# Performance work log

Measured on AMD Instinct MI355X. Metric: run time of the kernel, lower is better.

Reference implementation:

```python
import jax, jax.numpy as jnp
import numpy as np

B, T, NE, H = 4, 1024, 1024, 16
HS = NE // H  # 64
EPS = 0.00064


def setup_inputs() -> dict:
    key = jax.random.key(0)
    ks = jax.random.split(key, 30)
    def rn(k, shape, s):
        return jax.random.normal(k, shape, jnp.float32) * s
    d = {}
    d["x"] = jax.random.normal(ks[0], (B, T, NE), jnp.float32)
    d["time_maa_x"] = jax.random.uniform(ks[1], (NE,), jnp.float32)
    d["time_maa"] = jax.random.uniform(ks[2], (4, 1, 1, NE), jnp.float32)
    d["maa_w1"] = rn(ks[3], (128, NE), 0.02)   # 4 * D_MIX_LORA=32
    d["maa_w2"] = rn(ks[4], (4, 32, NE), 0.02)
    d["decay_w1"] = rn(ks[5], (64, NE), 0.02)
    d["decay_w2"] = rn(ks[6], (64, NE), 0.02)
    d["aaa_w1"] = rn(ks[7], (16, NE), 0.02)
    d["aaa_w2"] = rn(ks[8], (16, NE), 0.02)
    d["kkk_w1"] = rn(ks[9], (16, NE), 0.02)
    d["kkk_w2"] = rn(ks[10], (16, NE), 0.02)
    d["gate_w1"] = rn(ks[11], (128, NE), 0.02)
    d["gate_w2"] = rn(ks[12], (128, NE), 0.02)
    d["ma_w1"] = rn(ks[13], (16, NE), 0.02)
    d["ma_w2"] = rn(ks[14], (16, NE), 0.02)
    d["mk_w1"] = rn(ks[15], (16, NE), 0.02)
    d["mk_w2"] = rn(ks[16], (16, NE), 0.02)
    d["time_decay"] = jnp.linspace(-6.5, -1.5, NE, dtype=jnp.float32)  # decay_speed + 0.5 shape
    d["time_faaaa"] = rn(ks[17], (NE,), 0.02)
    d["time_aaaaa"] = rn(ks[18], (NE,), 0.02)
    d["time_misc_a"] = rn(ks[19], (NE,), 0.02)
    d["time_misc_k"] = rn(ks[20], (NE,), 0.02)
    d["Wr"] = rn(ks[21], (NE, NE), 0.5 / NE ** 0.5)
    d["Wk"] = rn(ks[22], (NE, NE), 0.05 / NE ** 0.5)
    d["Wv"] = rn(ks[23], (NE, NE), 0.5 / NE ** 0.5)
    d["Wo"] = rn(ks[24], (NE, NE), 1.0 / NE ** 0.5)
    d["ln_w"] = jnp.ones((NE,), jnp.float32)
    d["ln_b"] = jnp.zeros((NE,), jnp.float32)
    return d


def _forward(x, time_maa_x, time_maa, maa_w1, maa_w2, decay_w1, decay_w2,
             aaa_w1, aaa_w2, kkk_w1, kkk_w2, gate_w1, gate_w2,
             ma_w1, ma_w2, mk_w1, mk_w2, time_decay, time_faaaa, time_aaaaa,
             time_misc_a, time_misc_k, Wr, Wk, Wv, Wo, ln_w, ln_b):
    Bx, Tx, C = x.shape
    # token-shift delta: xx[t] = x[t-1] - x[t], with x[-1] = 0
    xx = jnp.pad(x, ((0, 0), (1, 0), (0, 0)))[:, :Tx] - x
    mix = x + xx * time_maa_x
    lo = jnp.tanh(jnp.einsum('btc,dc->btd', mix, maa_w1)).reshape(Bx, Tx, 4, 32)
    lo = jnp.einsum('btgk,gkc->gbtc', lo, maa_w2)           # [4,B,T,C]
    xm = x[None] + xx[None] * (lo + time_maa)               # time_maa broadcasts [4,1,1,C]
    xrg, xwa, xk, xv = xm[0], xm[1], xm[2], xm[3]

    r = xrg @ Wr.T
    g = jnp.tanh(xrg @ gate_w1.T) @ gate_w2
    k = xk @ Wk.T
    v = xv @ Wv.T
    w2 = jnp.tanh(xwa @ decay_w1.T) @ decay_w2
    w = -jax.nn.softplus(-(time_decay + w2)) - 0.5
    kk = k + jnp.tanh(xk @ kkk_w1.T) @ kkk_w2
    kkh = kk.reshape(Bx, Tx, H, HS)
    kk = (kkh / jnp.maximum(jnp.linalg.norm(kkh, axis=-1, keepdims=True), 1e-12)).reshape(Bx, Tx, C)
    a = jax.nn.sigmoid(time_aaaaa + (xwa @ aaa_w1.T) @ aaa_w2)
    ma = jax.nn.sigmoid(time_misc_a + (xwa @ ma_w1.T) @ ma_w2)
    k = k * ma + k * a * (1.0 - ma)
    mk = jax.nn.sigmoid(time_misc_k + (xk @ mk_w1.T) @ mk_w2)
    k = k * jnp.exp(w * mk)
    b = -kk * a

    # RWKV7 delta-rule recurrence: per-(B,H) HSxHS matrix state, scan over T
    def to_th(t):
        return t.reshape(Bx, Tx, H, HS).transpose(1, 0, 2, 3)  # [T,B,H,HS]
    qt, wt, kt, vt, at, bt = map(to_th, (r, w, k, v, kk, b))
    wt = jnp.exp(-jnp.exp(wt))

    def step(s, inp):
        q_, w_, k_, v_, a_, b_ = inp
        sa = jnp.einsum('bhij,bhj->bhi', s, a_)
        s = s * w_[:, :, None, :] + sa[..., None] * b_[:, :, None, :] + v_[..., None] * k_[:, :, None, :]
        return s, jnp.einsum('bhij,bhj->bhi', s, q_)

    s0 = jnp.zeros((Bx, H, HS, HS), x.dtype)
    _, y = jax.lax.scan(step, s0, (qt, wt, kt, vt, at, bt))
    y = y.transpose(1, 0, 2, 3).reshape(Bx, Tx, C)

    # GroupNorm with H groups, eps=0.00064
    yg = y.reshape(Bx, Tx, H, HS)
    mu = yg.mean(-1, keepdims=True)
    var = ((yg - mu) ** 2).mean(-1, keepdims=True)
    y = ((yg - mu) / jnp.sqrt(var + EPS)).reshape(Bx, Tx, C) * ln_w + ln_b

    # per-head bonus: (r.k * faaaa) v
    rk = (r.reshape(Bx, Tx, H, HS) * k.reshape(Bx, Tx, H, HS) * time_faaaa.reshape(H, HS)).sum(-1, keepdims=True)
    y = y + (rk * v.reshape(Bx, Tx, H, HS)).reshape(Bx, Tx, C)
    return (y * g) @ Wo.T


def reference(x, time_maa_x, time_maa, maa_w1, maa_w2, decay_w1, decay_w2,
              aaa_w1, aaa_w2, kkk_w1, kkk_w2, gate_w1, gate_w2,
              ma_w1, ma_w2, mk_w1, mk_w2, time_decay, time_faaaa, time_aaaaa,
              time_misc_a, time_misc_k, Wr, Wk, Wv, Wo, ln_w, ln_b):
    return _forward(x, time_maa_x, time_maa, maa_w1, maa_w2, decay_w1, decay_w2,
                    aaa_w1, aaa_w2, kkk_w1, kkk_w2, gate_w1, gate_w2,
                    ma_w1, ma_w2, mk_w1, mk_w2, time_decay, time_faaaa, time_aaaaa,
                    time_misc_a, time_misc_k, Wr, Wk, Wv, Wo, ln_w, ln_b)
```

## Files before the change

### kernel.cpp

```cpp
#include <hip/hip_runtime.h>
#include <cstdint>
#include <cstddef>

#define BB   4
#define TT   1024
#define CC   1024
#define HH   16
#define HSS  64
#define NNtok 4096
#define EPSGN 0.00064f
#define W2TS 192

typedef unsigned short bf16u;
typedef __attribute__((ext_vector_type(8))) short short8;
typedef __attribute__((ext_vector_type(4))) float f32x4;
#define SLOT 4194304ull

__device__ __forceinline__ float bf2f(bf16u u){
  union { unsigned int i; float f; } cv; cv.i = ((unsigned int)u) << 16; return cv.f;
}
__device__ __forceinline__ unsigned short f2bfbits(unsigned int x){
  return (unsigned short)((x + 0x7fffu + ((x >> 16) & 1u)) >> 16);
}
__device__ __forceinline__ bf16u f2bf(float f){
  union { float f; unsigned int i; } cv; cv.f = f;
  return f2bfbits(cv.i);
}
__device__ __forceinline__ void ld4bf(const bf16u* p, float* o){
  ushort4 u = *reinterpret_cast<const ushort4*>(p);
  o[0]=bf2f(u.x); o[1]=bf2f(u.y); o[2]=bf2f(u.z); o[3]=bf2f(u.w);
}
__device__ __forceinline__ void st4bf(bf16u* p, const float* v){
  ushort4 u; u.x=f2bf(v[0]); u.y=f2bf(v[1]); u.z=f2bf(v[2]); u.w=f2bf(v[3]);
  *reinterpret_cast<ushort4*>(p) = u;
}
__device__ __forceinline__ unsigned short f2h(float f){
  union { _Float16 h; unsigned short s; } c; c.h = (_Float16)f; return c.s;
}
__device__ __forceinline__ void st4h(bf16u* p, const float* v){
  ushort4 u; u.x=f2h(v[0]); u.y=f2h(v[1]); u.z=f2h(v[2]); u.w=f2h(v[3]);
  *reinterpret_cast<ushort4*>(p) = u;
}
__device__ __forceinline__ void ld4f(const float* p, float* o){
  float4 v = *reinterpret_cast<const float4*>(p);
  o[0]=v.x; o[1]=v.y; o[2]=v.z; o[3]=v.w;
}
__device__ __forceinline__ float sigm(float x){ return 1.f / (1.f + expf(-x)); }

__device__ __forceinline__ float bflo(unsigned int u){
  union { unsigned int i; float f; } c; c.i = u << 16; return c.f;
}
__device__ __forceinline__ float bfhi(unsigned int u){
  union { unsigned int i; float f; } c; c.i = u & 0xffff0000u; return c.f;
}
__device__ __forceinline__ float hlo(unsigned int u){
  union { unsigned short s; _Float16 h; } c; c.s = (unsigned short)(u & 0xffffu); return (float)c.h;
}
__device__ __forceinline__ float hhi(unsigned int u){
  union { unsigned short s; _Float16 h; } c; c.s = (unsigned short)(u >> 16); return (float)c.h;
}
__device__ __forceinline__ float hval(unsigned short s){
  union { unsigned short s; _Float16 h; } c; c.s = s; return (float)c.h;
}
__device__ __forceinline__ float dot4(const float* x, const float* y){
  return (x[0]*y[0] + x[1]*y[1]) + (x[2]*y[2] + x[3]*y[3]);
}

template<int CTRL>
__device__ __forceinline__ float dpp_add(float v){
  union { float f; int i; } a, b;
  a.f = v;
  b.i = __builtin_amdgcn_update_dpp(0, a.i, CTRL, 0xF, 0xF, true);
  return v + b.f;
}
__device__ __forceinline__ float red16(float v){
  v = dpp_add<0xB1>(v);
  v = dpp_add<0x4E>(v);
  v = dpp_add<0x124>(v);
  v = dpp_add<0x128>(v);
  return v;
}
__device__ __forceinline__ float red32(float v){
  v = red16(v);
  union { float f; int i; } x, y;
  x.f = v; y.f = v;
  asm volatile("" : "+v"(y.i));
  asm volatile("v_permlane16_swap_b32 %0, %1" : "+v"(x.i), "+v"(y.i));
  return x.f + y.f;
}

__global__ __launch_bounds__(256) void k_prep(const float* __restrict__ x,
                                              const float* __restrict__ tmx,
                                              bf16u* __restrict__ MIX){
  int e = (blockIdx.x * 256 + threadIdx.x) * 4;
  int n = e >> 10;
  int c = e & (CC - 1);
  int t = n & (TT - 1);
  float xf[4]; ld4f(x + e, xf);
  float pf[4] = {0.f, 0.f, 0.f, 0.f};
  if (t > 0) ld4f(x + e - CC, pf);
  float tm[4]; ld4f(tmx + c, tm);
  float mv[4];
  #pragma unroll
  for (int i = 0; i < 4; ++i) mv[i] = xf[i] + (pf[i] - xf[i]) * tm[i];
  st4bf(MIX + e, mv);
}

__global__ __launch_bounds__(256) void k_wconv1(
    const float* __restrict__ Wr, const float* __restrict__ Wk,
    const float* __restrict__ Wv,
    const float* __restrict__ maa_w1, const float* __restrict__ gate_w1,
    const float* __restrict__ decay_w1, const float* __restrict__ aaa_w1,
    const float* __restrict__ ma_w1, const float* __restrict__ kkk_w1,
    const float* __restrict__ mk_w1,
    const float* __restrict__ maa_w2, const float* __restrict__ decay_w2,
    bf16u* __restrict__ WrB, bf16u* __restrict__ WkB, bf16u* __restrict__ WvB,
    bf16u* __restrict__ W1B, bf16u* __restrict__ W2TB){
  int blk = blockIdx.x, tid = threadIdx.x;
  if (blk < 3072){
    const float* src = (blk < 1024) ? Wr : (blk < 2048) ? Wk : Wv;
    bf16u* dst = (blk < 1024) ? WrB : (blk < 2048) ? WkB : WvB;
    size_t e = (size_t)(blk & 1023) * 1024 + (size_t)tid * 4;
    float v[4]; ld4f(src + e, v);
    st4bf(dst + e, v);
  } else if (blk < 3456){
    int row = blk - 3072;
    const float* src;
    if      (row < 128) src = maa_w1   + (size_t)row * 1024;
    else if (row < 256) src = gate_w1  + (size_t)(row - 128) * 1024;
    else if (row < 320) src = decay_w1 + (size_t)(row - 256) * 1024;
    else if (row < 336) src = aaa_w1   + (size_t)(row - 320) * 1024;
    else if (row < 352) src = ma_w1    + (size_t)(row - 336) * 1024;
    else if (row < 368) src = kkk_w1   + (size_t)(row - 352) * 1024;
    else                src = mk_w1    + (size_t)(row - 368) * 1024;
    float v[4]; ld4f(src + tid * 4, v);
    st4bf(W1B + (size_t)row * 1024 + tid * 4, v);
  } else {
    int j = blk - 3456;
    const float* src = (j < 128) ? (maa_w2 + (size_t)j * 1024)
                                 : (decay_w2 + (size_t)(j - 128) * 1024);
    for (int c = tid; c < 1024; c += 256)
      W2TB[(size_t)c * W2TS + j] = f2bf(src[c]);
  }
}

__global__ __launch_bounds__(256) void k_wconv2(const float* __restrict__ Wo,
                                                const float* __restrict__ gate_w2,
                                                bf16u* __restrict__ WoB,
                                                bf16u* __restrict__ GW2T){
  int blk = blockIdx.x, tid = threadIdx.x;
  if (blk < 1024){
    size_t e = ((size_t)blk * 256 + tid) * 4;
    float v[4]; ld4f(Wo + e, v);
    st4bf(WoB + e, v);
  } else {
    int c = (blk - 1024) * 2 + (tid >> 7);
    int j = tid & 127;
    GW2T[(size_t)c * 128 + j] = f2bf(gate_w2[(size_t)j * CC + c]);
  }
}

#define B64_ASZ (64*40)
#define B64_BSZ (128*40)
template<bool OB>
__device__ __forceinline__ void gemm_b64_body(const bf16u* __restrict__ X,
                                              const bf16u* __restrict__ WB,
                                              void* __restrict__ OUTv,
                                              int Nd, int Kd, int act_n,
                                              short* __restrict__ As,
                                              short* __restrict__ Bs,
                                              int bn0, int bm0){
  const int tid  = threadIdx.x;
  const int lane = tid & 63;
  const int wv   = tid >> 6;
  const int wm   = wv >> 1, wn = wv & 1;
  const int l15  = lane & 15;
  const int quad = lane >> 4;

  f32x4 acc[2][4];
  #pragma unroll
  for (int mi = 0; mi < 2; ++mi)
    #pragma unroll
    for (int ni = 0; ni < 4; ++ni)
      #pragma unroll
      for (int rg = 0; rg < 4; ++rg) acc[mi][ni][rg] = 0.f;

  const int ra = tid >> 2, ka = (tid & 3) * 8;
  const int rb = tid >> 1, kb = (tid & 1) * 16;
  const bf16u* xsrc = X + (size_t)(bm0 + ra) * Kd;
  const bf16u* wsrc = (bn0 + rb < Nd) ? WB + (size_t)(bn0 + rb) * Kd : nullptr;

  uint4 xa = *(const uint4*)(xsrc + ka);
  uint4 wa = make_uint4(0,0,0,0), wb = wa;
  if (wsrc){
    wa = *(const uint4*)(wsrc + kb);
    wb = *(const uint4*)(wsrc + kb + 8);
  }
  *(uint4*)&As[ra * 40 + ka]      = xa;
  *(uint4*)&Bs[rb * 40 + kb]      = wa;
  *(uint4*)&Bs[rb * 40 + kb + 8]  = wb;
  __syncthreads();

  const int NK = Kd >> 5;
  for (int k = 0; k < NK; ++k){
    const int cur = k & 1;
    if (k + 1 < NK){
      int k0 = (k + 1) << 5;
      xa = *(const uint4*)(xsrc + k0 + ka);
      if (wsrc){
        wa = *(const uint4*)(wsrc + k0 + kb);
        wb = *(const uint4*)(wsrc + k0 + kb + 8);
      }
    }
    short8 af[2], bfg[4];
    #pragma unroll
    for (int mi = 0; mi < 2; ++mi)
      af[mi] = *(const short8*)&As[cur*B64_ASZ + (wm*32 + mi*16 + l15) * 40 + quad*8];
    #pragma unroll
    for (int ni = 0; ni < 4; ++ni)
      bfg[ni] = *(const short8*)&Bs[cur*B64_BSZ + (wn*64 + ni*16 + l15) * 40 + quad*8];
    #pragma unroll
    for (int mi = 0; mi < 2; ++mi)
      #pragma unroll
      for (int ni = 0; ni < 4; ++ni)
        acc[mi][ni] = __builtin_amdgcn_mfma_f32_16x16x32_bf16(af[mi], bfg[ni], acc[mi][ni], 0, 0, 0);
    if (k + 1 < NK){
      const int nxt = cur ^ 1;
      *(uint4*)&As[nxt*B64_ASZ + ra * 40 + ka]     = xa;
      *(uint4*)&Bs[nxt*B64_BSZ + rb * 40 + kb]     = wa;
      *(uint4*)&Bs[nxt*B64_BSZ + rb * 40 + kb + 8] = wb;
      __syncthreads();
    }
  }

  #pragma unroll
  for (int mi = 0; mi < 2; ++mi){
    #pragma unroll
    for (int ni = 0; ni < 4; ++ni){
      int col = bn0 + wn*64 + ni*16 + l15;
      if (col >= Nd) continue;
      #pragma unroll
      for (int rg = 0; rg < 4; ++rg){
        int row = bm0 + wm*32 + mi*16 + quad*4 + rg;
        float v = acc[mi][ni][rg];
        if (col < act_n) v = tanhf(v);
        if (OB) ((bf16u*)OUTv)[(size_t)row * Nd + col] = f2bf(v);
        else    ((float*)OUTv)[(size_t)row * Nd + col] = v;
      }
    }
  }
}

template<bool OB>
__global__ __launch_bounds__(256) void k_gemm_b64(const bf16u* __restrict__ X,
                                                  const bf16u* __restrict__ WB,
                                                  void* __restrict__ OUTv,
                                                  int Nd, int Kd, int act_n){
  __shared__ short As[2*B64_ASZ];
  __shared__ short Bs[2*B64_BSZ];
  gemm_b64_body<OB>(X, WB, OUTv, Nd, Kd, act_n, As, Bs,
                    blockIdx.x * 128, blockIdx.y * 64);
}

__global__ __launch_bounds__(256) void k_gemm_b64_lora(const bf16u* __restrict__ X0,
                                                       const bf16u* __restrict__ X1,
                                                       const bf16u* __restrict__ X2,
                                                       const bf16u* __restrict__ W1B,
                                                       bf16u* __restrict__ GT,
                                                       bf16u* __restrict__ P1,
                                                       bf16u* __restrict__ P2){
  __shared__ short As[2*B64_ASZ];
  __shared__ short Bs[2*B64_BSZ];
  const int z = blockIdx.z;
  const int bm0 = blockIdx.y * 64;
  if (z == 0)
    gemm_b64_body<true>(X0, W1B + 128*1024, GT, 128, CC, 128, As, Bs, 0, bm0);
  else if (z == 1)
    gemm_b64_body<true>(X1, W1B + 256*1024, P1, 96, CC, 64, As, Bs, 0, bm0);
  else
    gemm_b64_body<true>(X2, W1B + 352*1024, P2, 32, CC, 16, As, Bs, 0, bm0);
}

template<int KD, int EP>
__device__ __forceinline__ void gemm_nn_body(const bf16u* __restrict__ A, int lda,
                                             const bf16u* __restrict__ BT, int koff,
                                             bf16u* __restrict__ OUT,
                                             const float* __restrict__ x,
                                             const float* __restrict__ tma_g,
                                             short* __restrict__ As,
                                             short* __restrict__ Bs,
                                             int bn0, int bm0){
  const int tid  = threadIdx.x;
  const int lane = tid & 63;
  const int wv   = tid >> 6;
  const int wm   = wv >> 1, wn = wv & 1;
  const int l15  = lane & 15;
  const int quad = lane >> 4;

  for (int idx = tid; idx < 128 * (KD / 8); idx += 256){
    int r  = idx / (KD / 8);
    int kc = (idx % (KD / 8)) * 8;
    *(uint4*)&As[r * (KD + 8) + kc] =
        *(const uint4*)(A + (size_t)(bm0 + r) * lda + kc);
  }
  for (int idx = tid; idx < 128 * (KD / 8); idx += 256){
    int cc_ = idx / (KD / 8);
    int kc  = (idx % (KD / 8)) * 8;
    *(uint4*)&Bs[cc_ * (KD + 8) + kc] =
        *(const uint4*)(BT + (size_t)(bn0 + cc_) * W2TS + koff + kc);
  }
  __syncthreads();

  f32x4 acc[4][4];
  #pragma unroll
  for (int mi = 0; mi < 4; ++mi)
    #pragma unroll
    for (int ni = 0; ni < 4; ++ni)
      #pragma unroll
      for (int rg = 0; rg < 4; ++rg) acc[mi][ni][rg] = 0.f;

  #pragma unroll
  for (int kk = 0; kk < KD; kk += 32){
    short8 af[4], bfg[4];
    #pragma unroll
    for (int mi = 0; mi < 4; ++mi)
      af[mi] = *(const short8*)&As[(wm*64 + mi*16 + l15) * (KD + 8) + kk + quad*8];
    #pragma unroll
    for (int ni = 0; ni < 4; ++ni)
      bfg[ni] = *(const short8*)&Bs[(wn*64 + ni*16 + l15) * (KD + 8) + kk + quad*8];
    #pragma unroll
    for (int mi = 0; mi < 4; ++mi)
      #pragma unroll
      for (int ni = 0; ni < 4; ++ni)
        acc[mi][ni] = __builtin_amdgcn_mfma_f32_16x16x32_bf16(af[mi], bfg[ni], acc[mi][ni], 0, 0, 0);
  }

  #pragma unroll
  for (int mi = 0; mi < 4; ++mi){
    #pragma unroll
    for (int ni = 0; ni < 4; ++ni){
      int col = bn0 + wn*64 + ni*16 + l15;
      float tm = (EP == 1) ? tma_g[col] : 0.f;
      #pragma unroll
      for (int rg = 0; rg < 4; ++rg){
        int row = bm0 + wm*64 + mi*16 + quad*4 + rg;
        float v = acc[mi][ni][rg];
        if (EP == 1){
          float xv = x[(size_t)row * CC + col];
          float xp = ((row & (TT - 1)) == 0) ? 0.f : x[(size_t)row * CC + col - CC];
          v = xv + (xp - xv) * (v + tm);
        }
        OUT[(size_t)row * CC + col] = f2bf(v);
      }
    }
  }
}

template<int KD, int EP>
__global__ __launch_bounds__(256) void k_gemm_nn_b(const bf16u* __restrict__ A, int lda,
                                                   const bf16u* __restrict__ BT, int koff,
                                                   bf16u* __restrict__ OUT,
                                                   const float* __restrict__ x,
                                                   const float* __restrict__ tma_g){
  __shared__ short As[128 * (KD + 8)];
  __shared__ short Bs[128 * (KD + 8)];
  gemm_nn_body<KD, EP>(A, lda, BT, koff, OUT, x, tma_g, As, Bs,
                       blockIdx.x * 128, blockIdx.y * 128);
}

__global__ __launch_bounds__(256) void k_gemm_nn_b4(const bf16u* __restrict__ LO,
                                                    const bf16u* __restrict__ BT,
                                                    bf16u* __restrict__ X0base,
                                                    const float* __restrict__ x,
                                                    const float* __restrict__ tmaa){
  __shared__ short As[128 * 40];
  __shared__ short Bs[128 * 40];
  const int z = blockIdx.z;
  gemm_nn_body<32, 1>(LO + z*32, 128, BT, z*32, X0base + (size_t)z*SLOT,
                      x, tmaa + (size_t)z*CC, As, Bs,
                      blockIdx.x * 128, blockIdx.y * 128);
}

template<bool OB>
__global__ __launch_bounds__(256) void k_gemm_mfma(const bf16u* __restrict__ X,
                                                   const float* __restrict__ Wa,
                                                   const float* __restrict__ Wb,
                                                   const float* __restrict__ Wc,
                                                   int na, int nab,
                                                   void* __restrict__ OUTv,
                                                   int Nd, int Kd, int act_n){
  __shared__ short As[128 * 40];
  __shared__ short Bs[128 * 40];
  const int tid  = threadIdx.x;
  const int lane = tid & 63;
  const int wv   = tid >> 6;
  const int wm   = wv >> 1, wn = wv & 1;
  const int bn0  = blockIdx.x * 128;
  const int bm0  = blockIdx.y * 128;
  const int l15  = lane & 15;
  const int quad = lane >> 4;

  f32x4 acc[4][4];
  #pragma unroll
  for (int mi = 0; mi < 4; ++mi)
    #pragma unroll
    for (int ni = 0; ni < 4; ++ni)
      #pragma unroll
      for (int rg = 0; rg < 4; ++rg) acc[mi][ni][rg] = 0.f;

  const int r    = tid >> 1;
  const int half = (tid & 1) * 16;

  int rr = bn0 + r;
  const float* wsrc = nullptr;
  if (rr < na)        wsrc = Wa + (size_t)rr * Kd;
  else if (rr < nab)  wsrc = Wb + (size_t)(rr - na) * Kd;
  else if (rr < Nd)   wsrc = Wc + (size_t)(rr - nab) * Kd;
  const bf16u* xsrc = X + (size_t)(bm0 + r) * Kd;

  for (int k0 = 0; k0 < Kd; k0 += 32){
    uint4 xa = *(const uint4*)(xsrc + k0 + half);
    uint4 xb = *(const uint4*)(xsrc + k0 + half + 8);
    uint4 w0 = make_uint4(0,0,0,0), w1 = w0, w2 = w0, w3 = w0;
    if (wsrc){
      w0 = *(const uint4*)(wsrc + k0 + half);
      w1 = *(const uint4*)(wsrc + k0 + half + 4);
      w2 = *(const uint4*)(wsrc + k0 + half + 8);
      w3 = *(const uint4*)(wsrc + k0 + half + 12);
    }
    union { unsigned short s[8]; uint4 v; } p0, p1;
    p0.s[0]=f2bfbits(w0.x); p0.s[1]=f2bfbits(w0.y); p0.s[2]=f2bfbits(w0.z); p0.s[3]=f2bfbits(w0.w);
    p0.s[4]=f2bfbits(w1.x); p0.s[5]=f2bfbits(w1.y); p0.s[6]=f2bfbits(w1.z); p0.s[7]=f2bfbits(w1.w);
    p1.s[0]=f2bfbits(w2.x); p1.s[1]=f2bfbits(w2.y); p1.s[2]=f2bfbits(w2.z); p1.s[3]=f2bfbits(w2.w);
    p1.s[4]=f2bfbits(w3.x); p1.s[5]=f2bfbits(w3.y); p1.s[6]=f2bfbits(w3.z); p1.s[7]=f2bfbits(w3.w);

    *(uint4*)&As[r * 40 + half]     = xa;
    *(uint4*)&As[r * 40 + half + 8] = xb;
    *(uint4*)&Bs[r * 40 + half]     = p0.v;
    *(uint4*)&Bs[r * 40 + half + 8] = p1.v;
    __syncthreads();

    short8 af[4], bfg[4];
    #pragma unroll
    for (int mi = 0; mi < 4; ++mi)
      af[mi] = *(const short8*)&As[(wm*64 + mi*16 + l15) * 40 + quad*8];
    #pragma unroll
    for (int ni = 0; ni < 4; ++ni)
      bfg[ni] = *(const short8*)&Bs[(wn*64 + ni*16 + l15) * 40 + quad*8];
    #pragma unroll
    for (int mi = 0; mi < 4; ++mi)
      #pragma unroll
      for (int ni = 0; ni < 4; ++ni)
        acc[mi][ni] = __builtin_amdgcn_mfma_f32_16x16x32_bf16(af[mi], bfg[ni], acc[mi][ni], 0, 0, 0);
    __syncthreads();
  }

  #pragma unroll
  for (int mi = 0; mi < 4; ++mi){
    #pragma unroll
    for (int ni = 0; ni < 4; ++ni){
      int col = bn0 + wn*64 + ni*16 + l15;
      if (col >= Nd) continue;
      #pragma unroll
      for (int rg = 0; rg < 4; ++rg){
        int row = bm0 + wm*64 + mi*16 + quad*4 + rg;
        float v = acc[mi][ni][rg];
        if (col < act_n) v = tanhf(v);
        if (OB) ((bf16u*)OUTv)[(size_t)row * Nd + col] = f2bf(v);
        else    ((float*)OUTv)[(size_t)row * Nd + col] = v;
      }
    }
  }
}

template<int KD, int EP>
__global__ __launch_bounds__(256) void k_gemm_nn(const bf16u* __restrict__ A, int lda,
                                                 const float* __restrict__ B,
                                                 bf16u* __restrict__ OUT,
                                                 const float* __restrict__ x,
                                                 const float* __restrict__ tma_g){
  __shared__ short As[128 * (KD + 8)];
  __shared__ short Bs[128 * (KD + 8)];
  const int tid  = threadIdx.x;
  const int lane = tid & 63;
  const int wv   = tid >> 6;
  const int wm   = wv >> 1, wn = wv & 1;
  const int bn0  = blockIdx.x * 128;
  const int bm0  = blockIdx.y * 128;
  const int l15  = lane & 15;
  const int quad = lane >> 4;

  for (int idx = tid; idx < 128 * (KD / 8); idx += 256){
    int r  = idx / (KD / 8);
    int kc = (idx % (KD / 8)) * 8;
    *(uint4*)&As[r * (KD + 8) + kc] =
        *(const uint4*)(A + (size_t)(bm0 + r) * lda + kc);
  }
  for (int idx = tid; idx < KD * 128; idx += 256){
    int k = idx >> 7, c = idx & 127;
    Bs[c * (KD + 8) + k] = (short)f2bf(B[(size_t)k * CC + bn0 + c]);
  }
  __syncthreads();

  f32x4 acc[4][4];
  #pragma unroll
  for (int mi = 0; mi < 4; ++mi)
    #pragma unroll
    for (int ni = 0; ni < 4; ++ni)
      #pragma unroll
      for (int rg = 0; rg < 4; ++rg) acc[mi][ni][rg] = 0.f;

  #pragma unroll
  for (int kk = 0; kk < KD; kk += 32){
    short8 af[4], bfg[4];
    #pragma unroll
    for (int mi = 0; mi < 4; ++mi)
      af[mi] = *(const short8*)&As[(wm*64 + mi*16 + l15) * (KD + 8) + kk + quad*8];
    #pragma unroll
    for (int ni = 0; ni < 4; ++ni)
      bfg[ni] = *(const short8*)&Bs[(wn*64 + ni*16 + l15) * (KD + 8) + kk + quad*8];
    #pragma unroll
    for (int mi = 0; mi < 4; ++mi)
      #pragma unroll
      for (int ni = 0; ni < 4; ++ni)
        acc[mi][ni] = __builtin_amdgcn_mfma_f32_16x16x32_bf16(af[mi], bfg[ni], acc[mi][ni], 0, 0, 0);
  }

  #pragma unroll
  for (int mi = 0; mi < 4; ++mi){
    #pragma unroll
    for (int ni = 0; ni < 4; ++ni){
      int col = bn0 + wn*64 + ni*16 + l15;
      float tm = (EP == 1) ? tma_g[col] : 0.f;
      #pragma unroll
      for (int rg = 0; rg < 4; ++rg){
        int row = bm0 + wm*64 + mi*16 + quad*4 + rg;
        float v = acc[mi][ni][rg];
        if (EP == 1){
          float xv = x[(size_t)row * CC + col];
          float xp = ((row & (TT - 1)) == 0) ? 0.f : x[(size_t)row * CC + col - CC];
          v = xv + (xp - xv) * (v + tm);
        }
        OUT[(size_t)row * CC + col] = f2bf(v);
      }
    }
  }
}

template<int WMODE>
__global__ __launch_bounds__(256) void k_elem(bf16u* __restrict__ K0,
    const bf16u* __restrict__ P1, const bf16u* __restrict__ P2,
    const bf16u* __restrict__ W2A,
    const float* __restrict__ kw2, const float* __restrict__ aw2,
    const float* __restrict__ maw2, const float* __restrict__ mkw2,
    const float* __restrict__ td,  const float* __restrict__ taa,
    const float* __restrict__ tma, const float* __restrict__ tmk,
    const float* __restrict__ faaaa,
    bf16u* __restrict__ KKN, bf16u* __restrict__ Bb, bf16u* __restrict__ UX,
    float* __restrict__ WF,
    bf16u* __restrict__ Rq, float* __restrict__ Dsc, float* __restrict__ RKsc){
  int n0 = blockIdx.x * 4, tid = threadIdx.x;
  __shared__ float at_l[4][16], mat_l[4][16], kt_l[4][16], mkt_l[4][16];
  {
    int grp = tid >> 6, q = tid & 63, tt = q >> 4, j = q & 15;
    if (grp == 0)      at_l[tt][j]  = bf2f(P1[(size_t)(n0+tt)*96 + 64 + j]);
    else if (grp == 1) mat_l[tt][j] = bf2f(P1[(size_t)(n0+tt)*96 + 80 + j]);
    else if (grp == 2) kt_l[tt][j]  = bf2f(P2[(size_t)(n0+tt)*32 + j]);
    else               mkt_l[tt][j] = bf2f(P2[(size_t)(n0+tt)*32 + 16 + j]);
  }
  __syncthreads();
  int c  = tid * 4;
  int h  = tid >> 4;
  int lg = tid & 15;

  float kkk[4][4], aa[4][4], mam[4][4], mkm[4][4];
  #pragma unroll
  for (int tt = 0; tt < 4; ++tt)
    #pragma unroll
    for (int i = 0; i < 4; ++i){ kkk[tt][i]=0; aa[tt][i]=0; mam[tt][i]=0; mkm[tt][i]=0; }

  #pragma unroll 4
  for (int j = 0; j < 16; ++j){
    float wk[4], wa[4], wm[4], wq[4];
    ld4f(kw2  + (size_t)j*CC + c, wk);
    ld4f(aw2  + (size_t)j*CC + c, wa);
    ld4f(maw2 + (size_t)j*CC + c, wm);
    ld4f(mkw2 + (size_t)j*CC + c, wq);
    #pragma unroll
    for (int tt = 0; tt < 4; ++tt){
      float s1 = kt_l[tt][j], s2 = at_l[tt][j], s3 = mat_l[tt][j], s4 = mkt_l[tt][j];
      #pragma unroll
      for (int i = 0; i < 4; ++i){
        kkk[tt][i] += s1 * wk[i];
        aa[tt][i]  += s2 * wa[i];
        mam[tt][i] += s3 * wm[i];
        mkm[tt][i] += s4 * wq[i];
      }
    }
  }

  float td4[4], taa4[4], tma4[4], tmk4[4], fa4[4];
  ld4f(td + c, td4); ld4f(taa + c, taa4); ld4f(tma + c, tma4); ld4f(tmk + c, tmk4);
  ld4f(faaaa + c, fa4);

#define ELEM_TOKEN(TT_, E_, A_, B_, KF_, WD_) do{ \
    float k0a[4]; ld4bf(K0 + (E_), k0a); \
    float w2a[4]; ld4bf(W2A + (E_), w2a); \
    float ssq = 0.f; \
    _Pragma("unroll") \
    for (int i = 0; i < 4; ++i){ A_[i] = k0a[i] + kkk[TT_][i]; ssq += A_[i]*A_[i]; } \
    ssq = red16(ssq); \
    float rinv = 1.f / fmaxf(sqrtf(ssq), 1e-12f); \
    float outw_[4]; \
    _Pragma("unroll") \
    for (int i = 0; i < 4; ++i){ \
      float z  = td4[i] + w2a[i]; \
      float nz = -z; \
      float sp = (nz > 15.f) ? nz : log1pf(expf(nz)); \
      float w  = -sp - 0.5f; \
      float av  = sigm(taa4[i] + aa[TT_][i]); \
      float mav = sigm(tma4[i] + mam[TT_][i]); \
      float mkv = sigm(tmk4[i] + mkm[TT_][i]); \
      A_[i] *= rinv; \
      B_[i]  = -A_[i] * av; \
      KF_[i] = k0a[i] * (mav + av * (1.f - mav)) * expf(w * mkv); \
      float ou = -expf(w); \
      outw_[i] = ou; \
      if (WMODE == 1) WD_[i] = __expf(ou);               \
      else            WD_[i] = __expf(hval(f2h(ou)));    \
    } \
    st4bf(Bb + (E_), B_); \
    st4bf(K0 + (E_), KF_); \
    if (WMODE == 1) *(float4*)(WF + (E_)) = make_float4(WD_[0], WD_[1], WD_[2], WD_[3]); \
    else            st4h(UX + (E_), outw_); \
  }while(0)

  #pragma unroll
  for (int p = 0; p < 2; ++p){
    const int ttE = 2*p, ttO = ttE + 1;
    size_t eE = (size_t)(n0 + ttE) * CC + c;
    size_t eO = eE + CC;
    float aE[4], bE[4], kfE[4], wdE[4];
    float aO[4], bO[4], kfO[4], wdO[4];
    ELEM_TOKEN(ttE, eE, aE, bE, kfE, wdE);
    ELEM_TOKEN(ttO, eO, aO, bO, kfO, wdO);
    st4bf(KKN + eE, aE);

    float rE[4], rO[4];
    ld4bf(Rq + eE, rE); ld4bf(Rq + eO, rO);

    float rkE = red16(rE[0]*kfE[0]*fa4[0] + rE[1]*kfE[1]*fa4[1]
                    + rE[2]*kfE[2]*fa4[2] + rE[3]*kfE[3]*fa4[3]);
    float rkO = red16(rO[0]*kfO[0]*fa4[0] + rO[1]*kfO[1]*fa4[1]
                    + rO[2]*kfO[2]*fa4[2] + rO[3]*kfO[3]*fa4[3]);

    float c1 = red16(dot4(bE, aO));
    float d  = red16(dot4(kfE, aO));
    float u1[4];
    #pragma unroll
    for (int i = 0; i < 4; ++i) u1[i] = wdE[i]*aO[i] + c1*aE[i];
    st4bf(KKN + eO, u1);

    float cq = red16(dot4(bE, rE));
    float e1 = red16(dot4(kfE, rE));
    float qe[4];
    #pragma unroll
    for (int i = 0; i < 4; ++i) qe[i] = wdE[i]*rE[i] + cq*aE[i];
    st4bf(Rq + eE, qe);

    float cz  = red16(dot4(bO, rO));
    float e21 = red16(dot4(kfO, rO));
    float z[4];
    #pragma unroll
    for (int i = 0; i < 4; ++i) z[i] = wdO[i]*rO[i] + cz*aO[i];
    float cy  = red16(dot4(bE, z));
    float e20 = red16(dot4(kfE, z));
    float qo[4];
    #pragma unroll
    for (int i = 0; i < 4; ++i) qo[i] = wdE[i]*z[i] + cy*aE[i];
    st4bf(Rq + eO, qo);

    if (lg == 0){
      size_t pr = (size_t)((n0 + ttE) >> 1);
      float4 dv; dv.x = d; dv.y = e1; dv.z = e20; dv.w = e21;
      *(float4*)(Dsc + (pr * HH + h) * 4) = dv;
      RKsc[(size_t)(n0 + ttE) * HH + h] = rkE;
      RKsc[(size_t)(n0 + ttO) * HH + h] = rkO;
    }
  }
#undef ELEM_TOKEN
}

template<int WMODE>
__global__ __launch_bounds__(256) void k_rec(const bf16u* __restrict__ Qp,
                                             const bf16u* __restrict__ WT,
                                             const float* __restrict__ WF,
                                             const bf16u* __restrict__ KFt,
                                             const bf16u* __restrict__ Vt,
                                             const bf16u* __restrict__ Aa,
                                             const bf16u* __restrict__ Bv,
                                             const float* __restrict__ Dsc,
                                             bf16u* __restrict__ Y){
  const int p   = blockIdx.x;
  const int g   = (p & 7) | ((p >> 6) << 3);
  const int oct = (p >> 3) & 7;
  const int b   = g >> 4;
  const int h   = g & 15;
  const int tid = threadIdx.x;
  const int l31 = tid & 31;
  const int i   = oct * 8 + (tid >> 5);
  const size_t base0 = (size_t)(b * TT) * CC + h * HSS;
  const size_t colb  = base0 + l31 * 2;
  const size_t rowb  = base0 + i;
  const size_t dscb  = ((size_t)(b * (TT/2)) * HH + h) * 4;

  float S0 = 0.f, S1 = 0.f;

  unsigned int qEA,qOA,aEA,uOA,kEA,kOA,bEA,bOA,wEA,wOA; float2 fEA,fOA; unsigned short vEA,vOA; float4 dA;
  unsigned int qEB,qOB,aEB,uOB,kEB,kOB,bEB,bOB,wEB,wOB; float2 fEB,fOB; unsigned short vEB,vOB; float4 dB;
  unsigned int qEC,qOC,aEC,uOC,kEC,kOC,bEC,bOC,wEC,wOC; float2 fEC,fOC; unsigned short vEC,vOC; float4 dC;
  unsigned int qED,qOD,aED,uOD,kED,kOD,bED,bOD,wED,wOD; float2 fED,fOD; unsigned short vED,vOD; float4 dD;

#define PL(S, T_) do{ \
    size_t cE_ = colb + (size_t)(T_) * CC, cO_ = cE_ + CC; \
    qE##S = *(const unsigned int*)(Qp  + cE_); qO##S = *(const unsigned int*)(Qp  + cO_); \
    aE##S = *(const unsigned int*)(Aa  + cE_); uO##S = *(const unsigned int*)(Aa  + cO_); \
    kE##S = *(const unsigned int*)(KFt + cE_); kO##S = *(const unsigned int*)(KFt + cO_); \
    bE##S = *(const unsigned int*)(Bv  + cE_); bO##S = *(const unsigned int*)(Bv  + cO_); \
    if (WMODE == 1){ \
      fE##S = *(const float2*)(WF + cE_); fO##S = *(const float2*)(WF + cO_); \
    } else { \
      wE##S = *(const unsigned int*)(WT + cE_); wO##S = *(const unsigned int*)(WT + cO_); \
    } \
    vE##S = Vt[rowb + (size_t)(T_) * CC]; \
    vO##S = Vt[rowb + (size_t)(T_ + 1) * CC]; \
    d##S  = *(const float4*)(Dsc + dscb + (size_t)((T_) >> 1) * (HH*4)); \
  }while(0)

#define PSTEP(S, T_) do{ \
    float a0=bflo(aE##S), a1=bfhi(aE##S); \
    float u0=bflo(uO##S), u1=bfhi(uO##S); \
    float g0=bflo(qE##S), g1=bfhi(qE##S); \
    float o0=bflo(qO##S), o1=bfhi(qO##S); \
    float pE_ = fmaf(S1, a1, S0 * a0); \
    float pO_ = fmaf(S1, u1, S0 * u0); \
    float yE_ = fmaf(S1, g1, S0 * g0); \
    float yO_ = fmaf(S1, o1, S0 * o0); \
    pE_ = red32(pE_); \
    pO_ = red32(pO_); \
    yE_ = red32(yE_); \
    yO_ = red32(yO_); \
    float vEf = bf2f(vE##S), vOf = bf2f(vO##S); \
    float saE = pE_; \
    float saO = fmaf(d##S.x, vEf, pO_); \
    float ypE = fmaf(d##S.y, vEf, yE_); \
    float ypO = fmaf(d##S.z, vEf, fmaf(d##S.w, vOf, yO_)); \
    float k0=bflo(kE##S), k1=bfhi(kE##S); \
    float b0=bflo(bE##S), b1=bfhi(bE##S); \
    float w0, w1; \
    if (WMODE == 1){ w0=fE##S.x; w1=fE##S.y; } \
    else { w0=__expf(hlo(wE##S)); w1=__expf(hhi(wE##S)); } \
    S0 = fmaf(S0, w0, fmaf(saE, b0, vEf * k0)); \
    S1 = fmaf(S1, w1, fmaf(saE, b1, vEf * k1)); \
    float ko0=bflo(kO##S), ko1=bfhi(kO##S); \
    float bo0=bflo(bO##S), bo1=bfhi(bO##S); \
    float wo0, wo1; \
    if (WMODE == 1){ wo0=fO##S.x; wo1=fO##S.y; } \
    else { wo0=__expf(hlo(wO##S)); wo1=__expf(hhi(wO##S)); } \
    S0 = fmaf(S0, wo0, fmaf(saO, bo0, vOf * ko0)); \
    S1 = fmaf(S1, wo1, fmaf(saO, bo1, vOf * ko1)); \
    if (l31 == 0){ \
      Y[rowb + (size_t)(T_) * CC]     = f2bf(ypE); \
      Y[rowb + (size_t)(T_ + 1) * CC] = f2bf(ypO); \
    } \
  }while(0)

  PL(A, 0); PL(B, 2); PL(C, 4); PL(D, 6);
  for (int t = 0; t < TT; t += 8){
    PSTEP(A, t);
    if (t + 8  < TT) PL(A, t + 8);
    PSTEP(B, t + 2);
    if (t + 10 < TT) PL(B, t + 10);
    PSTEP(C, t + 4);
    if (t + 12 < TT) PL(C, t + 12);
    PSTEP(D, t + 6);
    if (t + 14 < TT) PL(D, t + 14);
  }
#undef PL
#undef PSTEP
}

__global__ __launch_bounds__(256) void k_post(const bf16u* __restrict__ Y,
                                              const bf16u* __restrict__ Vt,
                                              const bf16u* __restrict__ GV,
                                              const float* __restrict__ lnw,
                                              const float* __restrict__ lnb,
                                              const float* __restrict__ RKsc,
                                              bf16u* __restrict__ YG){
  int n = blockIdx.x, tid = threadIdx.x;
  int c = tid * 4;
  size_t e = (size_t)n * CC + c;

  float ya[4]; ld4bf(Y + e, ya);
  float s = ya[0] + ya[1] + ya[2] + ya[3];
  s = red16(s);
  float mu = s * (1.f / 64.f);
  float d[4], vs = 0.f;
  #pragma unroll
  for (int i = 0; i < 4; ++i){ d[i] = ya[i] - mu; vs += d[i] * d[i]; }
  vs = red16(vs);
  float rstd = rsqrtf(vs * (1.f / 64.f) + EPSGN);

  float rk = RKsc[(size_t)n * HH + (tid >> 4)];

  float va[4]; ld4bf(Vt + e, va);
  float lw4[4], lb4[4];
  ld4f(lnw + c, lw4); ld4f(lnb + c, lb4);
  float g[4]; ld4bf(GV + e, g);
  float o[4];
  #pragma unroll
  for (int i = 0; i < 4; ++i){
    float yn = d[i] * rstd * lw4[i] + lb4[i] + rk * va[i];
    o[i] = yn * g[i];
  }
  st4bf(YG + e, o);
}

extern "C" void kernel_launch(void* const* d_in, const int* in_sizes, int n_in,
                              void* d_out, int out_size, void* d_ws, size_t ws_size,
                              hipStream_t stream){
  (void)in_sizes; (void)n_in; (void)out_size;
  const float* x        = (const float*)d_in[0];
  const float* tmx      = (const float*)d_in[1];
  const float* tmaa     = (const float*)d_in[2];
  const float* maa_w1   = (const float*)d_in[3];
  const float* maa_w2   = (const float*)d_in[4];
  const float* decay_w1 = (const float*)d_in[5];
  const float* decay_w2 = (const float*)d_in[6];
  const float* aaa_w1   = (const float*)d_in[7];
  const float* aaa_w2   = (const float*)d_in[8];
  const float* kkk_w1   = (const float*)d_in[9];
  const float* kkk_w2   = (const float*)d_in[10];
  const float* gate_w1  = (const float*)d_in[11];
  const float* gate_w2  = (const float*)d_in[12];
  const float* ma_w1    = (const float*)d_in[13];
  const float* ma_w2    = (const float*)d_in[14];
  const float* mk_w1    = (const float*)d_in[15];
  const float* mk_w2    = (const float*)d_in[16];
  const float* t_decay  = (const float*)d_in[17];
  const float* t_faaaa  = (const float*)d_in[18];
  const float* t_aaaaa  = (const float*)d_in[19];
  const float* t_misc_a = (const float*)d_in[20];
  const float* t_misc_k = (const float*)d_in[21];
  const float* Wr       = (const float*)d_in[22];
  const float* Wk       = (const float*)d_in[23];
  const float* Wv       = (const float*)d_in[24];
  const float* Wo       = (const float*)d_in[25];
  const float* ln_w     = (const float*)d_in[26];
  const float* ln_b     = (const float*)d_in[27];

  bf16u* bw  = (bf16u*)d_ws;
  bf16u* MIX = bw + 0*SLOT;
  bf16u* X0  = bw + 0*SLOT;
  bf16u* KKN = bw + 0*SLOT;
  bf16u* YG  = bw + 0*SLOT;
  bf16u* X1  = bw + 1*SLOT;
  bf16u* Bb  = bw + 1*SLOT;
  bf16u* GV  = bw + 1*SLOT;
  bf16u* X2  = bw + 2*SLOT;
  bf16u* UX  = bw + 2*SLOT;
  bf16u* X3  = bw + 3*SLOT;
  bf16u* W2A = bw + 3*SLOT;
  bf16u* Yb  = bw + 3*SLOT;
  bf16u* R   = bw + 4*SLOT;
  bf16u* K0  = bw + 5*SLOT;
  bf16u* V   = bw + 6*SLOT;
  char*  wsb = (char*)d_ws;
  bf16u* LO  = (bf16u*)(wsb + (56ull<<20));
  bf16u* GT  = (bf16u*)(wsb + (57ull<<20));
  bf16u* P1  = (bf16u*)(wsb + (58ull<<20));
  bf16u* P2  = (bf16u*)(wsb + (58ull<<20) + (768ull<<10));
  float* Dsc = (float*)(wsb + (59ull<<20));
  float* RKsc= (float*)(wsb + (59ull<<20) + (512ull<<10));
  float* WF  = (float*)(wsb + (60ull<<20));
  bf16u* WrB = (bf16u*)(wsb + (60ull<<20));
  bf16u* WkB = (bf16u*)(wsb + (62ull<<20));
  bf16u* WvB = (bf16u*)(wsb + (64ull<<20));
  bf16u* W1B = (bf16u*)(wsb + (66ull<<20));
  bf16u* W2TB= (bf16u*)(wsb + (67ull<<20));
  bf16u* WoB = (bf16u*)(wsb + (60ull<<20));
  bf16u* GW2T= (bf16u*)(wsb + (62ull<<20));
  const bool fast = ws_size >= (77ull<<20);

  if (fast){
    k_wconv1<<<3648, 256, 0, stream>>>(Wr, Wk, Wv, maa_w1, gate_w1, decay_w1,
                                       aaa_w1, ma_w1, kkk_w1, mk_w1,
                                       maa_w2, decay_w2,
                                       WrB, WkB, WvB, W1B, W2TB);
    k_prep<<<4096, 256, 0, stream>>>(x, tmx, MIX);
    k_gemm_b64<true><<<dim3(1,64),256,0,stream>>>(MIX, W1B, LO, 128, CC, 128);
    k_gemm_nn_b4<<<dim3(8,32,4),256,0,stream>>>(LO, W2TB, X0, x, tmaa);
    k_gemm_b64<true><<<dim3(8,64),256,0,stream>>>(X0, WrB, R,  CC, CC, 0);
    k_gemm_b64<true><<<dim3(8,64),256,0,stream>>>(X2, WkB, K0, CC, CC, 0);
    k_gemm_b64<true><<<dim3(8,64),256,0,stream>>>(X3, WvB, V,  CC, CC, 0);
    k_gemm_b64_lora<<<dim3(1,64,3),256,0,stream>>>(X0, X1, X2, W1B, GT, P1, P2);
    k_gemm_nn_b<64,0><<<dim3(8,32),256,0,stream>>>(P1, 96, W2TB, 128, W2A, nullptr, nullptr);
    k_elem<1><<<1024, 256, 0, stream>>>(K0, P1, P2, W2A,
                                        kkk_w2, aaa_w2, ma_w2, mk_w2,
                                        t_decay, t_aaaaa, t_misc_a, t_misc_k, t_faaaa,
                                        KKN, Bb, UX, WF, R, Dsc, RKsc);
    k_rec<1><<<512, 256, 0, stream>>>(R, UX, WF, K0, V, KKN, Bb, Dsc, Yb);
    k_wconv2<<<1536, 256, 0, stream>>>(Wo, gate_w2, WoB, GW2T);
    k_gemm_b64<true><<<dim3(8,64),256,0,stream>>>(GT, GW2T, GV, CC, 128, 0);
    k_post<<<4096, 256, 0, stream>>>(Yb, V, GV, ln_w, ln_b, RKsc, YG);
    k_gemm_b64<false><<<dim3(8,64),256,0,stream>>>(YG, WoB, d_out, CC, CC, 0);
  } else {
    k_prep<<<4096, 256, 0, stream>>>(x, tmx, MIX);
    k_gemm_mfma<true><<<dim3(1,32),256,0,stream>>>(MIX, maa_w1, maa_w1, maa_w1,
                                                   128, 128, LO, 128, CC, 128);
    bf16u* XMs[4] = {X0, X1, X2, X3};
    for (int g = 0; g < 4; ++g)
      k_gemm_nn<32,1><<<dim3(8,32),256,0,stream>>>(LO + g*32, 128,
                                                   maa_w2 + (size_t)g*32*CC,
                                                   XMs[g], x, tmaa + (size_t)g*CC);
    k_gemm_mfma<true><<<dim3(8,32),256,0,stream>>>(X0, Wr, Wr, Wr, CC, CC, R,  CC, CC, 0);
    k_gemm_mfma<true><<<dim3(8,32),256,0,stream>>>(X2, Wk, Wk, Wk, CC, CC, K0, CC, CC, 0);
    k_gemm_mfma<true><<<dim3(8,32),256,0,stream>>>(X3, Wv, Wv, Wv, CC, CC, V,  CC, CC, 0);
    k_gemm_mfma<true><<<dim3(1,32),256,0,stream>>>(X0, gate_w1, gate_w1, gate_w1,
                                                   128, 128, GT, 128, CC, 128);
    k_gemm_mfma<true><<<dim3(1,32),256,0,stream>>>(X1, decay_w1, aaa_w1, ma_w1,
                                                   64, 80, P1, 96, CC, 64);
    k_gemm_mfma<true><<<dim3(1,32),256,0,stream>>>(X2, kkk_w1, mk_w1, mk_w1,
                                                   16, 32, P2, 32, CC, 16);
    k_gemm_nn<64,0><<<dim3(8,32),256,0,stream>>>(P1, 96, decay_w2, W2A, nullptr, nullptr);
    k_elem<0><<<1024, 256, 0, stream>>>(K0, P1, P2, W2A,
                                        kkk_w2, aaa_w2, ma_w2, mk_w2,
                                        t_decay, t_aaaaa, t_misc_a, t_misc_k, t_faaaa,
                                        KKN, Bb, UX, WF, R, Dsc, RKsc);
    k_rec<0><<<512, 256, 0, stream>>>(R, UX, WF, K0, V, KKN, Bb, Dsc, Yb);
    k_gemm_nn<128,0><<<dim3(8,32),256,0,stream>>>(GT, 128, gate_w2, GV, nullptr, nullptr);
    k_post<<<4096, 256, 0, stream>>>(Yb, V, GV, ln_w, ln_b, RKsc, YG);
    k_gemm_mfma<false><<<dim3(8,32),256,0,stream>>>(YG, Wo, Wo, Wo, CC, CC, d_out, CC, CC, 0);
  }
}
```

Measured before the change: 589.0 us.

## Deepen GEMM K-tile to 64, batch R/K/V GEMMs, fuse prep with weight conversion

```diff
diff --git a/kernel.cpp b/kernel.cpp
--- a/kernel.cpp
+++ b/kernel.cpp
@@ -106,7 +106,9 @@
   st4bf(MIX + e, mv);
 }
 
-__global__ __launch_bounds__(256) void k_wconv1(
+__global__ __launch_bounds__(256) void k_prep_wconv(
+    const float* __restrict__ x, const float* __restrict__ tmx,
+    bf16u* __restrict__ MIX,
     const float* __restrict__ Wr, const float* __restrict__ Wk,
     const float* __restrict__ Wv,
     const float* __restrict__ maa_w1, const float* __restrict__ gate_w1,
@@ -116,7 +118,23 @@
     const float* __restrict__ maa_w2, const float* __restrict__ decay_w2,
     bf16u* __restrict__ WrB, bf16u* __restrict__ WkB, bf16u* __restrict__ WvB,
     bf16u* __restrict__ W1B, bf16u* __restrict__ W2TB){
-  int blk = blockIdx.x, tid = threadIdx.x;
+  int tid = threadIdx.x;
+  if (blockIdx.x < 4096){
+    int e = (blockIdx.x * 256 + tid) * 4;
+    int n = e >> 10;
+    int c = e & (CC - 1);
+    int t = n & (TT - 1);
+    float xf[4]; ld4f(x + e, xf);
+    float pf[4] = {0.f, 0.f, 0.f, 0.f};
+    if (t > 0) ld4f(x + e - CC, pf);
+    float tm[4]; ld4f(tmx + c, tm);
+    float mv[4];
+    #pragma unroll
+    for (int i = 0; i < 4; ++i) mv[i] = xf[i] + (pf[i] - xf[i]) * tm[i];
+    st4bf(MIX + e, mv);
+    return;
+  }
+  int blk = blockIdx.x - 4096;
   if (blk < 3072){
     const float* src = (blk < 1024) ? Wr : (blk < 2048) ? Wk : Wv;
     bf16u* dst = (blk < 1024) ? WrB : (blk < 2048) ? WkB : WvB;
@@ -160,8 +178,9 @@
   }
 }
 
-#define B64_ASZ (64*40)
-#define B64_BSZ (128*40)
+#define B64_AROW 72
+#define B64_ASZ (64*72)
+#define B64_BSZ (128*72)
 template<bool OB>
 __device__ __forceinline__ void gemm_b64_body(const bf16u* __restrict__ X,
                                               const bf16u* __restrict__ WB,
@@ -185,50 +204,65 @@
       #pragma unroll
       for (int rg = 0; rg < 4; ++rg) acc[mi][ni][rg] = 0.f;
 
-  const int ra = tid >> 2, ka = (tid & 3) * 8;
-  const int rb = tid >> 1, kb = (tid & 1) * 16;
+  const int ra = tid >> 2, k0a = (tid & 3) * 16;
+  const int rb = tid >> 1, k0b = (tid & 1) * 32;
   const bf16u* xsrc = X + (size_t)(bm0 + ra) * Kd;
   const bf16u* wsrc = (bn0 + rb < Nd) ? WB + (size_t)(bn0 + rb) * Kd : nullptr;
 
-  uint4 xa = *(const uint4*)(xsrc + ka);
-  uint4 wa = make_uint4(0,0,0,0), wb = wa;
+  uint4 xa0 = *(const uint4*)(xsrc + k0a);
+  uint4 xa1 = *(const uint4*)(xsrc + k0a + 8);
+  uint4 wa0 = make_uint4(0,0,0,0), wa1 = wa0, wa2 = wa0, wa3 = wa0;
   if (wsrc){
-    wa = *(const uint4*)(wsrc + kb);
-    wb = *(const uint4*)(wsrc + kb + 8);
-  }
-  *(uint4*)&As[ra * 40 + ka]      = xa;
-  *(uint4*)&Bs[rb * 40 + kb]      = wa;
-  *(uint4*)&Bs[rb * 40 + kb + 8]  = wb;
+    wa0 = *(const uint4*)(wsrc + k0b);
+    wa1 = *(const uint4*)(wsrc + k0b + 8);
+    wa2 = *(const uint4*)(wsrc + k0b + 16);
+    wa3 = *(const uint4*)(wsrc + k0b + 24);
+  }
+  *(uint4*)&As[ra * B64_AROW + k0a]      = xa0;
+  *(uint4*)&As[ra * B64_AROW + k0a + 8]  = xa1;
+  *(uint4*)&Bs[rb * B64_AROW + k0b]      = wa0;
+  *(uint4*)&Bs[rb * B64_AROW + k0b + 8]  = wa1;
+  *(uint4*)&Bs[rb * B64_AROW + k0b + 16] = wa2;
+  *(uint4*)&Bs[rb * B64_AROW + k0b + 24] = wa3;
   __syncthreads();
 
-  const int NK = Kd >> 5;
-  for (int k = 0; k < NK; ++k){
-    const int cur = k & 1;
-    if (k + 1 < NK){
-      int k0 = (k + 1) << 5;
-      xa = *(const uint4*)(xsrc + k0 + ka);
+  const int NS = Kd >> 6;
+  for (int s = 0; s < NS; ++s){
+    const int cur = s & 1;
+    if (s + 1 < NS){
+      int kb = (s + 1) << 6;
+      xa0 = *(const uint4*)(xsrc + kb + k0a);
+      xa1 = *(const uint4*)(xsrc + kb + k0a + 8);
       if (wsrc){
-        wa = *(const uint4*)(wsrc + k0 + kb);
-        wb = *(const uint4*)(wsrc + k0 + kb + 8);
+        wa0 = *(const uint4*)(wsrc + kb + k0b);
+        wa1 = *(const uint4*)(wsrc + kb + k0b + 8);
+        wa2 = *(const uint4*)(wsrc + kb + k0b + 16);
+        wa3 = *(const uint4*)(wsrc + kb + k0b + 24);
       }
     }
-    short8 af[2], bfg[4];
-    #pragma unroll
-    for (int mi = 0; mi < 2; ++mi)
-      af[mi] = *(const short8*)&As[cur*B64_ASZ + (wm*32 + mi*16 + l15) * 40 + quad*8];
-    #pragma unroll
-    for (int ni = 0; ni < 4; ++ni)
-      bfg[ni] = *(const short8*)&Bs[cur*B64_BSZ + (wn*64 + ni*16 + l15) * 40 + quad*8];
-    #pragma unroll
-    for (int mi = 0; mi < 2; ++mi)
+    #pragma unroll
+    for (int kk = 0; kk < 64; kk += 32){
+      short8 af[2], bfg[4];
+      #pragma unroll
+      for (int mi = 0; mi < 2; ++mi)
+        af[mi] = *(const short8*)&As[cur*B64_ASZ + (wm*32 + mi*16 + l15) * B64_AROW + kk + quad*8];
       #pragma unroll
       for (int ni = 0; ni < 4; ++ni)
-        acc[mi][ni] = __builtin_amdgcn_mfma_f32_16x16x32_bf16(af[mi], bfg[ni], acc[mi][ni], 0, 0, 0);
-    if (k + 1 < NK){
+        bfg[ni] = *(const short8*)&Bs[cur*B64_BSZ + (wn*64 + ni*16 + l15) * B64_AROW + kk + quad*8];
+      #pragma unroll
+      for (int mi = 0; mi < 2; ++mi)
+        #pragma unroll
+        for (int ni = 0; ni < 4; ++ni)
+          acc[mi][ni] = __builtin_amdgcn_mfma_f32_16x16x32_bf16(af[mi], bfg[ni], acc[mi][ni], 0, 0, 0);
+    }
+    if (s + 1 < NS){
       const int nxt = cur ^ 1;
-      *(uint4*)&As[nxt*B64_ASZ + ra * 40 + ka]     = xa;
-      *(uint4*)&Bs[nxt*B64_BSZ + rb * 40 + kb]     = wa;
-      *(uint4*)&Bs[nxt*B64_BSZ + rb * 40 + kb + 8] = wb;
+      *(uint4*)&As[nxt*B64_ASZ + ra * B64_AROW + k0a]      = xa0;
+      *(uint4*)&As[nxt*B64_ASZ + ra * B64_AROW + k0a + 8]  = xa1;
+      *(uint4*)&Bs[nxt*B64_BSZ + rb * B64_AROW + k0b]      = wa0;
+      *(uint4*)&Bs[nxt*B64_BSZ + rb * B64_AROW + k0b + 8]  = wa1;
+      *(uint4*)&Bs[nxt*B64_BSZ + rb * B64_AROW + k0b + 16] = wa2;
+      *(uint4*)&Bs[nxt*B64_BSZ + rb * B64_AROW + k0b + 24] = wa3;
       __syncthreads();
     }
   }
@@ -260,6 +294,24 @@
   __shared__ short Bs[2*B64_BSZ];
   gemm_b64_body<OB>(X, WB, OUTv, Nd, Kd, act_n, As, Bs,
                     blockIdx.x * 128, blockIdx.y * 64);
+}
+
+__global__ __launch_bounds__(256) void k_gemm_b64_rkv(const bf16u* __restrict__ X0,
+                                                      const bf16u* __restrict__ X2,
+                                                      const bf16u* __restrict__ X3,
+                                                      const bf16u* __restrict__ WrB,
+                                                      const bf16u* __restrict__ WkB,
+                                                      const bf16u* __restrict__ WvB,
+                                                      bf16u* __restrict__ R,
+                                                      bf16u* __restrict__ K0,
+                                                      bf16u* __restrict__ V){
+  __shared__ short As[2*B64_ASZ];
+  __shared__ short Bs[2*B64_BSZ];
+  const int z = blockIdx.z;
+  const int bn0 = blockIdx.x * 128, bm0 = blockIdx.y * 64;
+  if (z == 0)      gemm_b64_body<true>(X0, WrB, R,  CC, CC, 0, As, Bs, bn0, bm0);
+  else if (z == 1) gemm_b64_body<true>(X2, WkB, K0, CC, CC, 0, As, Bs, bn0, bm0);
+  else             gemm_b64_body<true>(X3, WvB, V,  CC, CC, 0, As, Bs, bn0, bm0);
 }
 
 __global__ __launch_bounds__(256) void k_gemm_b64_lora(const bf16u* __restrict__ X0,
@@ -893,16 +945,15 @@
   const bool fast = ws_size >= (77ull<<20);
 
   if (fast){
-    k_wconv1<<<3648, 256, 0, stream>>>(Wr, Wk, Wv, maa_w1, gate_w1, decay_w1,
-                                       aaa_w1, ma_w1, kkk_w1, mk_w1,
-                                       maa_w2, decay_w2,
-                                       WrB, WkB, WvB, W1B, W2TB);
-    k_prep<<<4096, 256, 0, stream>>>(x, tmx, MIX);
+    k_prep_wconv<<<7744, 256, 0, stream>>>(x, tmx, MIX,
+                                           Wr, Wk, Wv, maa_w1, gate_w1, decay_w1,
+                                           aaa_w1, ma_w1, kkk_w1, mk_w1,
+                                           maa_w2, decay_w2,
+                                           WrB, WkB, WvB, W1B, W2TB);
     k_gemm_b64<true><<<dim3(1,64),256,0,stream>>>(MIX, W1B, LO, 128, CC, 128);
     k_gemm_nn_b4<<<dim3(8,32,4),256,0,stream>>>(LO, W2TB, X0, x, tmaa);
-    k_gemm_b64<true><<<dim3(8,64),256,0,stream>>>(X0, WrB, R,  CC, CC, 0);
-    k_gemm_b64<true><<<dim3(8,64),256,0,stream>>>(X2, WkB, K0, CC, CC, 0);
-    k_gemm_b64<true><<<dim3(8,64),256,0,stream>>>(X3, WvB, V,  CC, CC, 0);
+    k_gemm_b64_rkv<<<dim3(8,64,3),256,0,stream>>>(X0, X2, X3, WrB, WkB, WvB,
+                                                  R, K0, V);
     k_gemm_b64_lora<<<dim3(1,64,3),256,0,stream>>>(X0, X1, X2, W1B, GT, P1, P2);
     k_gemm_nn_b<64,0><<<dim3(8,32),256,0,stream>>>(P1, 96, W2TB, 128, W2A, nullptr, nullptr);
     k_elem<1><<<1024, 256, 0, stream>>>(K0, P1, P2, W2A,
```

Measured after the change: 566.4 us (median of 2 runs). 1.04x faster.
